# Kernel tuning notes

Measured on AMD Instinct MI355X. Metric: run time of the kernel, lower is better.

Reference implementation:

```python
import jax, jax.numpy as jnp
import numpy as np

N_NODES = 50000
N_EDGES = 800000
D = 128
BN_EPS = 1e-5


def swish(h):
    return h * jax.nn.sigmoid(h)


def linear_bn_swish(h, W, b, g, be):
    # Linear -> BatchNorm1d (training stats, biased var) -> Swish
    h = h @ W + b
    mean = jnp.mean(h, axis=0)
    var = jnp.mean((h - mean) ** 2, axis=0)
    h = (h - mean) * jax.lax.rsqrt(var + BN_EPS) * g + be
    return swish(h)


def setup_inputs() -> dict:
    key = jax.random.key(0)
    ks = jax.random.split(key, 8)
    scale = 1.0 / np.sqrt(D)
    return {
        "x": jax.random.normal(ks[0], (N_NODES, D), dtype=jnp.float32),
        "vals": jax.random.uniform(ks[1], (N_EDGES,), dtype=jnp.float32),
        "W1": jax.random.normal(ks[2], (D, D), dtype=jnp.float32) * scale,
        "b1": jnp.zeros((D,), dtype=jnp.float32),
        "g1": jnp.ones((D,), dtype=jnp.float32),
        "be1": jnp.zeros((D,), dtype=jnp.float32),
        "W2": jax.random.normal(ks[3], (D, D), dtype=jnp.float32) * scale,
        "b2": jnp.zeros((D,), dtype=jnp.float32),
        "g2": jnp.ones((D,), dtype=jnp.float32),
        "be2": jnp.zeros((D,), dtype=jnp.float32),
        "eps": jnp.zeros((1,), dtype=jnp.float32),
        "rows": jax.random.randint(ks[4], (N_EDGES,), 0, N_NODES, dtype=jnp.int32),
        "cols": jax.random.randint(ks[5], (N_EDGES,), 0, N_NODES, dtype=jnp.int32),
    }


def reference(x, vals, W1, b1, g1, be1, W2, b2, g2, be2, eps, rows, cols):
    # out = spmm(adj, x): gather neighbor features, scale by edge weight, scatter-add to rows
    msgs = vals[:, None] * x[cols]                                   # [E, D]
    agg = jax.ops.segment_sum(msgs, rows, num_segments=x.shape[0])   # [N, D]
    h = agg + (1.0 + eps[0]) * x
    h = linear_bn_swish(h, W1, b1, g1, be1)
    h = linear_bn_swish(h, W2, b2, g2, be2)
    return h
```

## Files before the change

### kernel.cpp

```cpp
#include <hip/hip_runtime.h>

#define D 128
#define DH 64
#define BR 64
#define BSH 6
#define NBMAX 1024
#define FCAP 2048
#define GT 512
#define CH 4096
#define SCT 512
#define TS 68

typedef float f32x4 __attribute__((ext_vector_type(4)));
typedef short s16x8 __attribute__((ext_vector_type(8)));

static __device__ __forceinline__ unsigned short f2bf(float f) {
    unsigned u = __float_as_uint(f);
    u += 0x7FFF + ((u >> 16) & 1);
    return (unsigned short)(u >> 16);
}
static __device__ __forceinline__ float bflo(unsigned u) { return __uint_as_float(u << 16); }
static __device__ __forceinline__ float bfhi(unsigned u) { return __uint_as_float(u & 0xFFFF0000u); }
static __device__ __forceinline__ float bf2f(short v) {
    return __uint_as_float(((unsigned)(unsigned short)v) << 16);
}

__global__ __launch_bounds__(256)
void k_setup(const float* __restrict__ x, unsigned* __restrict__ xh, int total4,
             const float* __restrict__ W1, const float* __restrict__ W2,
             unsigned short* __restrict__ Wsw1, unsigned short* __restrict__ Wsw2,
             int* __restrict__ ccur, float* __restrict__ stats, int eb) {
    int bid = blockIdx.x, t = threadIdx.x;
    if (bid < eb) {
        int i = bid * 256 + t;
        if (i < total4) {
            float4 v = ((const float4*)x)[i];
            uint2 o;
            o.x = (unsigned)f2bf(v.x) | ((unsigned)f2bf(v.y) << 16);
            o.y = (unsigned)f2bf(v.z) | ((unsigned)f2bf(v.w) << 16);
            ((uint2*)xh)[i] = o;
        }
    } else if (bid < eb + 16) {
        int gidx = (bid - eb) * 256 + t;
        const float* W = (gidx < 2048) ? W1 : W2;
        unsigned short* Wsw = (gidx < 2048) ? Wsw1 : Wsw2;
        int idx = gidx & 2047;
        int lane = idx & 63, nt = (idx >> 6) & 7, kt = idx >> 9;
        int k0 = kt * 32 + (lane >> 4) * 8;
        int n = nt * 16 + (lane & 15);
        unsigned short* dst = &Wsw[(size_t)((kt * 8 + nt) * 64 + lane) * 8];
#pragma unroll
        for (int j = 0; j < 8; ++j) dst[j] = f2bf(W[(k0 + j) * D + n]);
    } else {
        if (t < 512) stats[t] = 0.f;
        for (int i = t; i < NBMAX; i += 256) ccur[i] = 0;
    }
}

__global__ __launch_bounds__(SCT)
void k_cscatter(const int* __restrict__ rows, const int* __restrict__ cols,
                const float* __restrict__ vals, int* __restrict__ gcur,
                uint2* __restrict__ sedge, int E, int chunk) {
    __shared__ int lcnt[NBMAX];
    __shared__ int lbase[NBMAX];
    __shared__ int gbase[NBMAX];
    __shared__ uint2 sl[CH];
    __shared__ unsigned short sbkt[CH];
    int t = threadIdx.x;
    int base = blockIdx.x * chunk;
    int tot = min(E - base, chunk);
    if (tot <= 0) return;

    for (int i = t; i < NBMAX; i += SCT) lcnt[i] = 0;
    __syncthreads();

    int r[8]; unsigned c[8], v[8];
#pragma unroll
    for (int j = 0; j < 8; ++j) {
        int o = j * SCT + t;
        if (o < tot) {
            int e = base + o;
            r[j] = rows[e];
            c[j] = (unsigned)cols[e];
            v[j] = __float_as_uint(vals[e]);
            atomicAdd(&lcnt[r[j] >> BSH], 1);
        } else r[j] = -1;
    }
    __syncthreads();

    if (t < 64) {
        int part[16], s = 0;
#pragma unroll
        for (int k = 0; k < 16; ++k) {
            part[k] = s;
            s += lcnt[t * 16 + k];
        }
        int incl = s;
#pragma unroll
        for (int d = 1; d < 64; d <<= 1) {
            int n = __shfl_up(incl, d, 64);
            if (t >= d) incl += n;
        }
        int excl = incl - s;
#pragma unroll
        for (int k = 0; k < 16; ++k) lbase[t * 16 + k] = excl + part[k];
    }
    __syncthreads();

    for (int i = t; i < NBMAX; i += SCT) {
        int cnt = lcnt[i];
        gbase[i] = cnt ? atomicAdd(&gcur[i], cnt) : 0;
        lcnt[i] = 0;
    }
    __syncthreads();

#pragma unroll
    for (int j = 0; j < 8; ++j) {
        if (r[j] >= 0) {
            int b = r[j] >> BSH;
            int p = lbase[b] + atomicAdd(&lcnt[b], 1);
            sl[p] = make_uint2(c[j] | ((unsigned)(r[j] & (BR - 1)) << 16), v[j]);
            sbkt[p] = (unsigned short)b;
        }
    }
    __syncthreads();

#pragma unroll
    for (int j = 0; j < 8; ++j) {
        int i = j * SCT + t;
        if (i < tot) {
            int b = sbkt[i];
            int pos = gbase[b] + (i - lbase[b]);
            if (pos < FCAP) sedge[(size_t)b * FCAP + pos] = sl[i];
        }
    }
}

__global__ __launch_bounds__(GT, 6)
void k_sgg(const uint2* __restrict__ sedge, const int* __restrict__ ccur,
           const unsigned* __restrict__ xh, const float* __restrict__ eps,
           const unsigned short* __restrict__ Wsw, const float* __restrict__ bias,
           unsigned short* __restrict__ Hout, float* __restrict__ stats, int N) {
    __shared__ int cnt[BR], sbase[BR], cur[BR];
    __shared__ __align__(16) unsigned char uAbuf[64 * TS * 4];
    __shared__ uint2 ebufB[FCAP];
    __shared__ float redS[8 * 64];
    __shared__ float redQ[8 * 64];
    uint2* ebufA = (uint2*)uAbuf;
    unsigned* tile = (unsigned*)uAbuf;

    int b = blockIdx.x, t = threadIdx.x;
    size_t e0 = (size_t)b * FCAP;
    int cntE = ccur[b];
    if (cntE > FCAP) cntE = FCAP;
    if (t < BR) { cnt[t] = 0; cur[t] = 0; }
    __syncthreads();
    for (int i = t; i < cntE; i += GT) {
        uint2 ed = sedge[e0 + i];
        ebufA[i] = ed;
        atomicAdd(&cnt[ed.x >> 16], 1);
    }
    __syncthreads();
    if (t < BR) sbase[t] = cnt[t];
    __syncthreads();
    for (int d = 1; d < BR; d <<= 1) {
        int add = (t < BR && t >= d) ? sbase[t - d] : 0;
        __syncthreads();
        if (t < BR) sbase[t] += add;
        __syncthreads();
    }
    if (t < BR) sbase[t] -= cnt[t];
    __syncthreads();
    for (int i = t; i < cntE; i += GT) {
        uint2 ed = ebufA[i];
        int r = ed.x >> 16;
        int p = sbase[r] + atomicAdd(&cur[r], 1);
        ebufB[p] = make_uint2(ed.x & 0xFFFFu, ed.y);
    }
    __syncthreads();

    int lane = t & 63, w = t >> 6;
    float s = 1.0f + eps[0];
    int row0 = b * BR;
    for (int rl = w; rl < BR; rl += 8) {
        int grow = row0 + rl;
        if (grow >= N) { tile[rl * TS + lane] = 0; continue; }
        unsigned u = xh[(size_t)grow * DH + lane];
        float ax = s * bflo(u), ay = s * bfhi(u);
        int i0 = sbase[rl];
        int i1 = (rl < BR - 1) ? sbase[rl + 1] : cntE;
        for (int i = i0; i < i1; i += 16) {
            unsigned uu[16]; float vv[16];
#pragma unroll
            for (int j = 0; j < 16; ++j) {
                int idx = (i + j < i1) ? (i + j) : (i1 - 1);
                uint2 ed = ebufB[idx];
                vv[j] = (i + j < i1) ? __uint_as_float(ed.y) : 0.f;
                uu[j] = xh[(size_t)ed.x * DH + lane];
            }
#pragma unroll
            for (int j = 0; j < 16; ++j) {
                ax += vv[j] * bflo(uu[j]);
                ay += vv[j] * bfhi(uu[j]);
            }
        }
        tile[rl * TS + lane] = (unsigned)f2bf(ax) | ((unsigned)f2bf(ay) << 16);
    }
    __syncthreads();

    int m = lane & 15, quad = lane >> 4;
    int wr = w & 3, wc = w >> 2;
    int arowl = wr * 16 + m;

    f32x4 acc[4];
#pragma unroll
    for (int ntl = 0; ntl < 4; ++ntl) acc[ntl] = (f32x4){0.f, 0.f, 0.f, 0.f};

    const s16x8* wp = (const s16x8*)Wsw;
#pragma unroll
    for (int kt = 0; kt < 4; ++kt) {
        s16x8 a = *(const s16x8*)&tile[arowl * TS + kt * 16 + quad * 4];
#pragma unroll
        for (int ntl = 0; ntl < 4; ++ntl) {
            int nt = wc * 4 + ntl;
            s16x8 bf = wp[(kt * 8 + nt) * 64 + lane];
            acc[ntl] = __builtin_amdgcn_mfma_f32_16x16x32_bf16(a, bf, acc[ntl], 0, 0, 0);
        }
    }

#pragma unroll
    for (int ntl = 0; ntl < 4; ++ntl) {
        int nt = wc * 4 + ntl;
        float bv = bias[nt * 16 + m];
        float ss = 0.f, q = 0.f;
#pragma unroll
        for (int r = 0; r < 4; ++r) {
            int row = row0 + wr * 16 + quad * 4 + r;
            float h = acc[ntl][r] + bv;
            if (row < N) {
                Hout[(size_t)row * D + nt * 16 + m] = f2bf(h);
                ss += h; q += h * h;
            }
        }
        ss += __shfl_xor(ss, 16, 64); ss += __shfl_xor(ss, 32, 64);
        q += __shfl_xor(q, 16, 64);   q += __shfl_xor(q, 32, 64);
        if (quad == 0) {
            redS[w * 64 + ntl * 16 + m] = ss;
            redQ[w * 64 + ntl * 16 + m] = q;
        }
    }
    __syncthreads();
    if (t < D) {
        int ch = t >> 6, cl = t & 63;
        float ts = 0.f, tq = 0.f;
#pragma unroll
        for (int wr2 = 0; wr2 < 4; ++wr2) {
            ts += redS[(ch * 4 + wr2) * 64 + cl];
            tq += redQ[(ch * 4 + wr2) * 64 + cl];
        }
        atomicAdd(&stats[t], ts);
        atomicAdd(&stats[D + t], tq);
    }
}

__global__ __launch_bounds__(256)
void k_gemm2f(const unsigned short* __restrict__ H1, const unsigned short* __restrict__ Wsw,
              const float* __restrict__ bias, const float* __restrict__ stats1,
              const float* __restrict__ g1, const float* __restrict__ be1, float invN,
              unsigned short* __restrict__ Hout, float* __restrict__ stats2, int N) {
    __shared__ float redS[4 * D];
    __shared__ float redQ[4 * D];
    __shared__ float sa[D], sb[D];
    int tid = threadIdx.x, lane = tid & 63, w = tid >> 6;
    if (tid < D) {
        float mean = stats1[tid] * invN;
        float var = fmaxf(stats1[D + tid] * invN - mean * mean, 0.f);
        float a = g1[tid] * rsqrtf(var + 1e-5f);
        sa[tid] = a;
        sb[tid] = be1[tid] - mean * a;
    }
    __syncthreads();

    int row0 = blockIdx.x * 64 + w * 16;
    int m = lane & 15, quad = lane >> 4;

    f32x4 acc[8];
#pragma unroll
    for (int nt = 0; nt < 8; ++nt) acc[nt] = (f32x4){0.f, 0.f, 0.f, 0.f};

    int arow = row0 + m;
    bool avalid = arow < N;
    const s16x8* wp = (const s16x8*)Wsw;
    s16x8 az = {0, 0, 0, 0, 0, 0, 0, 0};
#pragma unroll
    for (int kt = 0; kt < 4; ++kt) {
        s16x8 a = az;
        if (avalid) {
            s16x8 raw = *(const s16x8*)&H1[(size_t)arow * D + kt * 32 + quad * 8];
#pragma unroll
            for (int j = 0; j < 8; ++j) {
                int k = kt * 32 + quad * 8 + j;
                float dd = bf2f(raw[j]) * sa[k] + sb[k];
                float o = dd / (1.f + __expf(-dd));
                a[j] = (short)f2bf(o);
            }
        }
#pragma unroll
        for (int nt = 0; nt < 8; ++nt) {
            s16x8 b = wp[(kt * 8 + nt) * 64 + lane];
            acc[nt] = __builtin_amdgcn_mfma_f32_16x16x32_bf16(a, b, acc[nt], 0, 0, 0);
        }
    }

#pragma unroll
    for (int nt = 0; nt < 8; ++nt) {
        float bv = bias[nt * 16 + m];
        float s = 0.f, q = 0.f;
#pragma unroll
        for (int r = 0; r < 4; ++r) {
            int row = row0 + quad * 4 + r;
            float h = acc[nt][r] + bv;
            if (row < N) {
                Hout[(size_t)row * D + nt * 16 + m] = f2bf(h);
                s += h; q += h * h;
            }
        }
        s += __shfl_xor(s, 16, 64); s += __shfl_xor(s, 32, 64);
        q += __shfl_xor(q, 16, 64); q += __shfl_xor(q, 32, 64);
        if (quad == 0) {
            redS[w * D + nt * 16 + m] = s;
            redQ[w * D + nt * 16 + m] = q;
        }
    }
    __syncthreads();
    if (tid < D) {
        float ts = redS[tid] + redS[D + tid] + redS[2 * D + tid] + redS[3 * D + tid];
        float tq = redQ[tid] + redQ[D + tid] + redQ[2 * D + tid] + redQ[3 * D + tid];
        atomicAdd(&stats2[tid], ts);
        atomicAdd(&stats2[D + tid], tq);
    }
}

__global__ void k_bnswish(const unsigned* __restrict__ inh, float* __restrict__ outp,
                          const float* __restrict__ stats, const float* __restrict__ g,
                          const float* __restrict__ be, float invN, int total4) {
    __shared__ float sa[D], sb[D];
    int j = threadIdx.x;
    if (j < D) {
        float mean = stats[j] * invN;
        float var = fmaxf(stats[D + j] * invN - mean * mean, 0.f);
        float a = g[j] * rsqrtf(var + 1e-5f);
        sa[j] = a;
        sb[j] = be[j] - mean * a;
    }
    __syncthreads();
    int i = blockIdx.x * blockDim.x + threadIdx.x;
    if (i >= total4) return;
    uint2 u = ((const uint2*)inh)[i];
    int c = (i * 4) & (D - 1);
    float d0 = bflo(u.x) * sa[c + 0] + sb[c + 0];
    float d1 = bfhi(u.x) * sa[c + 1] + sb[c + 1];
    float d2 = bflo(u.y) * sa[c + 2] + sb[c + 2];
    float d3 = bfhi(u.y) * sa[c + 3] + sb[c + 3];
    float o0 = d0 / (1.f + __expf(-d0));
    float o1 = d1 / (1.f + __expf(-d1));
    float o2 = d2 / (1.f + __expf(-d2));
    float o3 = d3 / (1.f + __expf(-d3));
    ((float4*)outp)[i] = make_float4(o0, o1, o2, o3);
}

extern "C" void kernel_launch(void* const* d_in, const int* in_sizes, int n_in,
                              void* d_out, int out_size, void* d_ws, size_t ws_size,
                              hipStream_t stream) {
    const float* x    = (const float*)d_in[0];
    const float* vals = (const float*)d_in[1];
    const float* W1   = (const float*)d_in[2];
    const float* b1   = (const float*)d_in[3];
    const float* g1   = (const float*)d_in[4];
    const float* be1  = (const float*)d_in[5];
    const float* W2   = (const float*)d_in[6];
    const float* b2   = (const float*)d_in[7];
    const float* g2   = (const float*)d_in[8];
    const float* be2  = (const float*)d_in[9];
    const float* eps  = (const float*)d_in[10];
    const int*  rows  = (const int*)d_in[11];
    const int*  cols  = (const int*)d_in[12];
    float* out = (float*)d_out;

    int N = in_sizes[0] / D;
    int E = in_sizes[1];
    int nb = (N + BR - 1) / BR;

    char* p = (char*)d_ws;
    float* stats = (float*)p;              p += 4 * D * sizeof(float);
    int* ccur = (int*)p;                   p += (size_t)NBMAX * sizeof(int);
    p = (char*)(((uintptr_t)p + 15) & ~(uintptr_t)15);
    unsigned short* Wsw1 = (unsigned short*)p; p += (size_t)D * D * 2;
    unsigned short* Wsw2 = (unsigned short*)p; p += (size_t)D * D * 2;
    p = (char*)(((uintptr_t)p + 15) & ~(uintptr_t)15);
    uint2* sedge  = (uint2*)p;             p += (size_t)nb * FCAP * sizeof(uint2);
    unsigned* xh = (unsigned*)p;           p += (size_t)N * DH * sizeof(unsigned);
    unsigned* h1 = (unsigned*)p;

    float* stats1 = stats;
    float* stats2 = stats + 2 * D;

    int total4 = N * D / 4;
    int eb = (total4 + 255) / 256;
    int gblk = (N + 63) / 64;
    float invN = 1.0f / (float)N;
    int scb = 256;
    int chunk = (E + scb - 1) / scb;
    if (chunk > CH) { scb = (E + CH - 1) / CH; chunk = (E + scb - 1) / scb; }

    k_setup<<<eb + 17, 256, 0, stream>>>(x, xh, total4, W1, W2, Wsw1, Wsw2,
                                         ccur, stats, eb);
    k_cscatter<<<scb, SCT, 0, stream>>>(rows, cols, vals, ccur, sedge, E, chunk);
    k_sgg<<<nb, GT, 0, stream>>>(sedge, ccur, xh, eps, Wsw1, b1,
                                 (unsigned short*)h1, stats1, N);
    k_gemm2f<<<gblk, 256, 0, stream>>>((const unsigned short*)h1, Wsw2, b2,
                                       stats1, g1, be1, invN,
                                       (unsigned short*)xh, stats2, N);
    k_bnswish<<<eb, 256, 0, stream>>>(xh, out, stats2, g2, be2, invN, total4);
}
```

Measured before the change: 223.7 us.

## Fuse second BN+swish into GEMM2 via grid-wide barrier; retune gather loop

The second GEMM kernel now stays resident after computing its tile and its column statistics. It waits on a global atomic counter until every block has contributed its stats, then applies BN2 and swish directly from the accumulators and writes fp32 output. This removes the bf16 intermediate write, its re-read, and one kernel launch. The grid barrier assumes all 782 blocks are co-resident (launch_bounds 256,4 over the CUs), otherwise it deadlocks. Separately, the SpMM gather loop moves from 16-wide predicated batches to 8-wide unpredicated batches with a scalar tail, and k_sgg's occupancy hint rises from 6 to 8.

Measured after the change: 322.2 us. 44.1% more time.

```diff
diff --git a/kernel.cpp b/kernel.cpp
--- a/kernel.cpp
+++ b/kernel.cpp
@@ -29,7 +29,8 @@
 void k_setup(const float* __restrict__ x, unsigned* __restrict__ xh, int total4,
              const float* __restrict__ W1, const float* __restrict__ W2,
              unsigned short* __restrict__ Wsw1, unsigned short* __restrict__ Wsw2,
-             int* __restrict__ ccur, float* __restrict__ stats, int eb) {
+             int* __restrict__ ccur, float* __restrict__ stats,
+             unsigned* __restrict__ done, int eb) {
     int bid = blockIdx.x, t = threadIdx.x;
     if (bid < eb) {
         int i = bid * 256 + t;
@@ -54,6 +55,7 @@
     } else {
         if (t < 512) stats[t] = 0.f;
         for (int i = t; i < NBMAX; i += 256) ccur[i] = 0;
+        if (t == 0) *done = 0u;
     }
 }
 
@@ -136,7 +138,7 @@
     }
 }
 
-__global__ __launch_bounds__(GT, 6)
+__global__ __launch_bounds__(GT, 8)
 void k_sgg(const uint2* __restrict__ sedge, const int* __restrict__ ccur,
            const unsigned* __restrict__ xh, const float* __restrict__ eps,
            const unsigned short* __restrict__ Wsw, const float* __restrict__ bias,
@@ -187,22 +189,28 @@
         if (grow >= N) { tile[rl * TS + lane] = 0; continue; }
         unsigned u = xh[(size_t)grow * DH + lane];
         float ax = s * bflo(u), ay = s * bfhi(u);
-        int i0 = sbase[rl];
+        int i = sbase[rl];
         int i1 = (rl < BR - 1) ? sbase[rl + 1] : cntE;
-        for (int i = i0; i < i1; i += 16) {
-            unsigned uu[16]; float vv[16];
-#pragma unroll
-            for (int j = 0; j < 16; ++j) {
-                int idx = (i + j < i1) ? (i + j) : (i1 - 1);
-                uint2 ed = ebufB[idx];
-                vv[j] = (i + j < i1) ? __uint_as_float(ed.y) : 0.f;
-                uu[j] = xh[(size_t)ed.x * DH + lane];
+        for (; i + 8 <= i1; i += 8) {
+            uint2 ed[8];
+            unsigned uu[8];
+#pragma unroll
+            for (int j = 0; j < 8; ++j) ed[j] = ebufB[i + j];
+#pragma unroll
+            for (int j = 0; j < 8; ++j) uu[j] = xh[(size_t)ed[j].x * DH + lane];
+#pragma unroll
+            for (int j = 0; j < 8; ++j) {
+                float v = __uint_as_float(ed[j].y);
+                ax += v * bflo(uu[j]);
+                ay += v * bfhi(uu[j]);
             }
-#pragma unroll
-            for (int j = 0; j < 16; ++j) {
-                ax += vv[j] * bflo(uu[j]);
-                ay += vv[j] * bfhi(uu[j]);
-            }
+        }
+        for (; i < i1; ++i) {
+            uint2 ed = ebufB[i];
+            unsigned uu = xh[(size_t)ed.x * DH + lane];
+            float v = __uint_as_float(ed.y);
+            ax += v * bflo(uu);
+            ay += v * bfhi(uu);
         }
         tile[rl * TS + lane] = (unsigned)f2bf(ax) | ((unsigned)f2bf(ay) << 16);
     }
@@ -263,11 +271,13 @@
     }
 }
 
-__global__ __launch_bounds__(256)
-void k_gemm2f(const unsigned short* __restrict__ H1, const unsigned short* __restrict__ Wsw,
-              const float* __restrict__ bias, const float* __restrict__ stats1,
-              const float* __restrict__ g1, const float* __restrict__ be1, float invN,
-              unsigned short* __restrict__ Hout, float* __restrict__ stats2, int N) {
+__global__ __launch_bounds__(256, 4)
+void k_gemm2fb(const unsigned short* __restrict__ H1, const unsigned short* __restrict__ Wsw,
+               const float* __restrict__ bias, const float* __restrict__ stats1,
+               const float* __restrict__ g1, const float* __restrict__ be1,
+               const float* __restrict__ g2, const float* __restrict__ be2, float invN,
+               float* __restrict__ outp, float* __restrict__ stats2,
+               unsigned* __restrict__ done, int N, int nblk) {
     __shared__ float redS[4 * D];
     __shared__ float redQ[4 * D];
     __shared__ float sa[D], sb[D];
@@ -320,10 +330,7 @@
         for (int r = 0; r < 4; ++r) {
             int row = row0 + quad * 4 + r;
             float h = acc[nt][r] + bv;
-            if (row < N) {
-                Hout[(size_t)row * D + nt * 16 + m] = f2bf(h);
-                s += h; q += h * h;
-            }
+            if (row < N) { s += h; q += h * h; }
         }
         s += __shfl_xor(s, 16, 64); s += __shfl_xor(s, 32, 64);
         q += __shfl_xor(q, 16, 64); q += __shfl_xor(q, 32, 64);
@@ -339,34 +346,43 @@
         atomicAdd(&stats2[tid], ts);
         atomicAdd(&stats2[D + tid], tq);
     }
-}
-
-__global__ void k_bnswish(const unsigned* __restrict__ inh, float* __restrict__ outp,
-                          const float* __restrict__ stats, const float* __restrict__ g,
-                          const float* __restrict__ be, float invN, int total4) {
-    __shared__ float sa[D], sb[D];
-    int j = threadIdx.x;
-    if (j < D) {
-        float mean = stats[j] * invN;
-        float var = fmaxf(stats[D + j] * invN - mean * mean, 0.f);
-        float a = g[j] * rsqrtf(var + 1e-5f);
-        sa[j] = a;
-        sb[j] = be[j] - mean * a;
-    }
-    __syncthreads();
-    int i = blockIdx.x * blockDim.x + threadIdx.x;
-    if (i >= total4) return;
-    uint2 u = ((const uint2*)inh)[i];
-    int c = (i * 4) & (D - 1);
-    float d0 = bflo(u.x) * sa[c + 0] + sb[c + 0];
-    float d1 = bfhi(u.x) * sa[c + 1] + sb[c + 1];
-    float d2 = bflo(u.y) * sa[c + 2] + sb[c + 2];
-    float d3 = bfhi(u.y) * sa[c + 3] + sb[c + 3];
-    float o0 = d0 / (1.f + __expf(-d0));
-    float o1 = d1 / (1.f + __expf(-d1));
-    float o2 = d2 / (1.f + __expf(-d2));
-    float o3 = d3 / (1.f + __expf(-d3));
-    ((float4*)outp)[i] = make_float4(o0, o1, o2, o3);
+    __threadfence();
+    __syncthreads();
+
+    if (tid == 0) {
+        atomicAdd(done, 1u);
+        while (atomicAdd(done, 0u) < (unsigned)nblk)
+            __builtin_amdgcn_s_sleep(8);
+    }
+    __syncthreads();
+    __threadfence();
+
+    if (tid < D) {
+        float s1 = atomicAdd(&stats2[tid], 0.f);
+        float s2 = atomicAdd(&stats2[D + tid], 0.f);
+        float mean = s1 * invN;
+        float var = fmaxf(s2 * invN - mean * mean, 0.f);
+        float a = g2[tid] * rsqrtf(var + 1e-5f);
+        sa[tid] = a;
+        sb[tid] = be2[tid] - mean * a;
+    }
+    __syncthreads();
+
+#pragma unroll
+    for (int nt = 0; nt < 8; ++nt) {
+        float bv = bias[nt * 16 + m];
+        float aa = sa[nt * 16 + m];
+        float bb = sb[nt * 16 + m];
+#pragma unroll
+        for (int r = 0; r < 4; ++r) {
+            int row = row0 + quad * 4 + r;
+            if (row < N) {
+                float h = acc[nt][r] + bv;
+                float dd = h * aa + bb;
+                outp[(size_t)row * D + nt * 16 + m] = dd / (1.f + __expf(-dd));
+            }
+        }
+    }
 }
 
 extern "C" void kernel_launch(void* const* d_in, const int* in_sizes, int n_in,
@@ -394,6 +410,7 @@
     char* p = (char*)d_ws;
     float* stats = (float*)p;              p += 4 * D * sizeof(float);
     int* ccur = (int*)p;                   p += (size_t)NBMAX * sizeof(int);
+    unsigned* done = (unsigned*)p;         p += 16;
     p = (char*)(((uintptr_t)p + 15) & ~(uintptr_t)15);
     unsigned short* Wsw1 = (unsigned short*)p; p += (size_t)D * D * 2;
     unsigned short* Wsw2 = (unsigned short*)p; p += (size_t)D * D * 2;
@@ -414,12 +431,11 @@
     if (chunk > CH) { scb = (E + CH - 1) / CH; chunk = (E + scb - 1) / scb; }
 
     k_setup<<<eb + 17, 256, 0, stream>>>(x, xh, total4, W1, W2, Wsw1, Wsw2,
-                                         ccur, stats, eb);
+                                         ccur, stats, done, eb);
     k_cscatter<<<scb, SCT, 0, stream>>>(rows, cols, vals, ccur, sedge, E, chunk);
     k_sgg<<<nb, GT, 0, stream>>>(sedge, ccur, xh, eps, Wsw1, b1,
                                  (unsigned short*)h1, stats1, N);
-    k_gemm2f<<<gblk, 256, 0, stream>>>((const unsigned short*)h1, Wsw2, b2,
-                                       stats1, g1, be1, invN,
-                                       (unsigned short*)xh, stats2, N);
-    k_bnswish<<<eb, 256, 0, stream>>>(xh, out, stats2, g2, be2, invN, total4);
-}
+    k_gemm2fb<<<gblk, 256, 0, stream>>>((const unsigned short*)h1, Wsw2, b2,
+                                        stats1, g1, be1, g2, be2, invN,
+                                        out, stats2, done, N, gblk);
+}
```
